# Performance work log

Measured on AMD Instinct MI355X. Metric: run time of the kernel, lower is better.

Reference implementation:

```python
import jax, jax.numpy as jnp
import numpy as np


def conv1x1(x, W, b):
    # x: [B, Cin, H, W], W: [Cout, Cin], b: [Cout] -> [B, Cout, H, W]
    return jnp.einsum('bchw,oc->bohw', x, W) + b[None, :, None, None]


def setup_inputs() -> dict:
    key = jax.random.key(0)
    ks = jax.random.split(key, 10)
    B, C, H, W = 16, 512, 64, 64
    c = C // 8  # in_ch // scale
    s_in = 1.0 / np.sqrt(C)
    s_c = 1.0 / np.sqrt(c)
    return {
        'x': jax.random.normal(ks[0], (B, C, H, W), dtype=jnp.float32),
        'Wq': jax.random.normal(ks[1], (c, C), dtype=jnp.float32) * s_in,
        'bq': jax.random.normal(ks[2], (c,), dtype=jnp.float32) * 0.01,
        'Wk': jax.random.normal(ks[3], (c, C), dtype=jnp.float32) * s_in,
        'bk': jax.random.normal(ks[4], (c,), dtype=jnp.float32) * 0.01,
        'Wv': jax.random.normal(ks[5], (c, C), dtype=jnp.float32) * s_in,
        'bv': jax.random.normal(ks[6], (c,), dtype=jnp.float32) * 0.01,
        'Wo': jax.random.normal(ks[7], (C, c), dtype=jnp.float32) * s_c,
        'bo': jax.random.normal(ks[8], (C,), dtype=jnp.float32) * 0.01,
        'gamma': jax.random.uniform(ks[9], (1,), dtype=jnp.float32),
    }


def reference(x, Wq, bq, Wk, bk, Wv, bv, Wo, bo, gamma):
    B, C, H, W = x.shape
    c = Wq.shape[0]
    N = H * W
    queries = conv1x1(x, Wq, bq).reshape(B, c, N)          # [B, c, N]
    # NOTE: original torch code does .view(-1, h*w, c): a pure reshape of the
    # contiguous [B, c, N] buffer, NOT a transpose. Reproduce exactly.
    keys = conv1x1(x, Wk, bk).reshape(B, N, c)             # [B, N, c] (reshape!)
    attn = jax.nn.softmax(jnp.einsum('bcn,bnd->bcd', queries, keys), axis=-1)  # [B, c, c]
    values = conv1x1(x, Wv, bv).reshape(B, c, N)           # [B, c, N]
    out = jnp.einsum('bcd,bdn->bcn', attn, values).reshape(B, c, H, W)
    out = conv1x1(out, Wo, bo)                             # [B, C, H, W]
    return out * gamma + x
```

## Files before the change

### kernel.cpp

```cpp
#include <hip/hip_runtime.h>

typedef unsigned short ushortT;
typedef unsigned int uintT;
typedef __attribute__((ext_vector_type(8))) short short8;
typedef __attribute__((ext_vector_type(4))) short short4v;
typedef __attribute__((ext_vector_type(4))) float float4v;

constexpr int B  = 16;
constexpr int C  = 512;
constexpr int CC = 64;
constexpr int N  = 4096;

constexpr size_t QK_OFF  = 0;
constexpr size_t S_OFF   = 8388608;
constexpr size_t VT_OFF  = 8454144;
constexpr size_t MF_OFF  = 10551296;
constexpr size_t WH_OFF  = 10813440;
constexpr size_t WL_OFF  = 10862592;
constexpr size_t WOT_OFF = 10911744;
constexpr size_t SP_OFF  = 10944512;

#define GLL(lds, g) __builtin_amdgcn_global_load_lds( \
    (const __attribute__((address_space(1))) void*)(g), \
    (__attribute__((address_space(3))) void*)(lds), 16, 0, 0)

static __device__ __forceinline__ ushortT f2bf(float f) {
    uintT u = __float_as_uint(f);
    u = (u + 0x7fffu + ((u >> 16) & 1u)) >> 16;
    return (ushortT)u;
}
static __device__ __forceinline__ float bf2f(ushortT h) {
    return __uint_as_float(((uintT)h) << 16);
}

__global__ __launch_bounds__(256) void k_prep_w(
    const float* __restrict__ Wq, const float* __restrict__ Wk,
    const float* __restrict__ Wv, const float* __restrict__ Wo,
    ushortT* __restrict__ wh, ushortT* __restrict__ wl, float* __restrict__ wot)
{
    int idx = blockIdx.x * 256 + threadIdx.x;
    if (idx < 3 * CC * C) {
        int m = idx >> 9, k = idx & 511;
        const float* W = (m < 64) ? Wq : (m < 128 ? Wk : Wv);
        float v = W[(m & 63) * C + k];
        ushortT h = f2bf(v);
        ushortT l = f2bf(v - bf2f(h));
        int kt = k >> 6, kk = k & 63;
        size_t off = ((size_t)(kt * 192 + m)) * 64 + (size_t)(((kk >> 3) ^ (m & 7)) * 8) + (kk & 7);
        wh[off] = h;
        wl[off] = l;
    } else {
        int i2 = idx - 3 * CC * C;
        int cc = i2 >> 9, co = i2 & 511;
        wot[i2] = Wo[co * CC + cc];
    }
}

__global__ __launch_bounds__(256) void k_qkv(
    const float* __restrict__ x,
    const ushortT* __restrict__ wh, const ushortT* __restrict__ wl,
    const float* __restrict__ bq, const float* __restrict__ bk,
    const float* __restrict__ bv,
    float* __restrict__ qk, ushortT* __restrict__ vt)
{
    __shared__ ushortT Ah[192 * 64];
    __shared__ ushortT Al[192 * 64];
    __shared__ ushortT Bh[2][64 * 64];
    __shared__ ushortT Bl[2][64 * 64];

    const int tid  = threadIdx.x;
    const int n0   = blockIdx.x * 64;
    const int b    = blockIdx.y;
    const int lane = tid & 63;
    const int wv   = tid >> 6;
    const int L15  = lane & 15, Lq = lane >> 4;

    const int nl  = tid & 63;
    const int kg0 = tid >> 6;

    const float* xb = x + (size_t)b * C * N + n0 + nl;

    float xr[2][8];
    float4v acc[3][4];
    const float4v vzero = {0.f, 0.f, 0.f, 0.f};
#pragma unroll
    for (int mi = 0; mi < 3; ++mi)
#pragma unroll
        for (int ni = 0; ni < 4; ++ni) acc[mi][ni] = vzero;

#pragma unroll
    for (int u = 0; u < 2; ++u) {
        const int kg = kg0 + 4 * u;
#pragma unroll
        for (int j = 0; j < 8; ++j)
            xr[u][j] = xb[(size_t)(kg * 8 + j) * N];
    }
    {
        const char* srcH = (const char*)wh;
        const char* srcL = (const char*)wl;
#pragma unroll
        for (int i = 0; i < 6; ++i) {
            int off = i * 4096 + tid * 16;
            GLL((char*)Ah + off, srcH + off);
            GLL((char*)Al + off, srcL + off);
        }
    }
#pragma unroll
    for (int u = 0; u < 2; ++u) {
        const int kg = kg0 + 4 * u;
        short8 h8, l8;
#pragma unroll
        for (int j = 0; j < 8; ++j) {
            float v = xr[u][j];
            ushortT h = f2bf(v);
            h8[j] = (short)h;
            l8[j] = (short)f2bf(v - bf2f(h));
        }
        int idx = nl * 64 + (kg ^ (nl & 7)) * 8;
        *(short8*)&Bh[0][idx] = h8;
        *(short8*)&Bl[0][idx] = l8;
    }
    __syncthreads();

    for (int kt = 0; kt < 8; ++kt) {
        const int cur = kt & 1;
        if (kt < 7) {
#pragma unroll
            for (int u = 0; u < 2; ++u) {
                const int kg = kg0 + 4 * u;
#pragma unroll
                for (int j = 0; j < 8; ++j)
                    xr[u][j] = xb[(size_t)((kt + 1) * 64 + kg * 8 + j) * N];
            }
        }
#pragma unroll
        for (int s = 0; s < 2; ++s) {
            short8 fbh[4], fbl[4];
#pragma unroll
            for (int ni = 0; ni < 4; ++ni) {
                int row = ni * 16 + L15;
                int off = row * 64 + ((4 * s + Lq) ^ (row & 7)) * 8;
                fbh[ni] = *(const short8*)&Bh[cur][off];
                fbl[ni] = *(const short8*)&Bl[cur][off];
            }
#pragma unroll
            for (int mi = 0; mi < 3; ++mi) {
                int rm = 48 * wv + mi * 16 + L15;
                int aoff = rm * 64 + ((4 * s + Lq) ^ (rm & 7)) * 8;
                short8 ah = *(const short8*)&Ah[aoff];
                short8 al = *(const short8*)&Al[aoff];
#pragma unroll
                for (int ni = 0; ni < 4; ++ni)
                    acc[mi][ni] = __builtin_amdgcn_mfma_f32_16x16x32_bf16(ah, fbh[ni], acc[mi][ni], 0, 0, 0);
#pragma unroll
                for (int ni = 0; ni < 4; ++ni)
                    acc[mi][ni] = __builtin_amdgcn_mfma_f32_16x16x32_bf16(al, fbh[ni], acc[mi][ni], 0, 0, 0);
#pragma unroll
                for (int ni = 0; ni < 4; ++ni)
                    acc[mi][ni] = __builtin_amdgcn_mfma_f32_16x16x32_bf16(ah, fbl[ni], acc[mi][ni], 0, 0, 0);
            }
        }
        __syncthreads();
        if (kt < 7) {
            const char* srcH = (const char*)wh + (size_t)(kt + 1) * 24576;
            const char* srcL = (const char*)wl + (size_t)(kt + 1) * 24576;
#pragma unroll
            for (int i = 0; i < 6; ++i) {
                int off = i * 4096 + tid * 16;
                GLL((char*)Ah + off, srcH + off);
                GLL((char*)Al + off, srcL + off);
            }
            const int nxt = cur ^ 1;
#pragma unroll
            for (int u = 0; u < 2; ++u) {
                const int kg = kg0 + 4 * u;
                short8 h8, l8;
#pragma unroll
                for (int j = 0; j < 8; ++j) {
                    float v = xr[u][j];
                    ushortT h = f2bf(v);
                    h8[j] = (short)h;
                    l8[j] = (short)f2bf(v - bf2f(h));
                }
                int idx = nl * 64 + (kg ^ (nl & 7)) * 8;
                *(short8*)&Bh[nxt][idx] = h8;
                *(short8*)&Bl[nxt][idx] = l8;
            }
            __syncthreads();
        }
    }

#pragma unroll
    for (int mi = 0; mi < 3; ++mi) {
        int rbase = 48 * wv + mi * 16;
        int type = rbase >> 6;
#pragma unroll
        for (int ni = 0; ni < 4; ++ni) {
            int col = n0 + ni * 16 + L15;
            float4v v4 = acc[mi][ni];
            if (type == 0) {
#pragma unroll
                for (int reg = 0; reg < 4; ++reg) {
                    int rl = (rbase + Lq * 4 + reg) & 63;
                    qk[((size_t)(b * 64 + rl)) * N + col] = v4[reg] + bq[rl];
                }
            } else if (type == 1) {
#pragma unroll
                for (int reg = 0; reg < 4; ++reg) {
                    int rl = (rbase + Lq * 4 + reg) & 63;
                    qk[((size_t)((16 + b) * 64 + rl)) * N + col] = v4[reg] + bk[rl];
                }
            } else {
                int rl0 = (rbase + Lq * 4) & 63;
                short4v p;
#pragma unroll
                for (int reg = 0; reg < 4; ++reg)
                    p[reg] = (short)f2bf(v4[reg] + bv[rl0 + reg]);
                size_t off = ((size_t)(b * N + col)) * 64 + (size_t)(((rl0 >> 3) ^ (col & 7)) * 8) + (rl0 & 7);
                *(short4v*)&vt[off] = p;
            }
        }
    }
}

__global__ __launch_bounds__(256) void k_logits(
    const float* __restrict__ qk, float* __restrict__ Sp)
{
    int b    = blockIdx.x;
    int part = blockIdx.y;
    __shared__ float Qs[64 * 68];
    __shared__ float Ks[64 * 64];

    const float* Qb = qk + (size_t)b * (CC * N);
    const float* Kb = qk + (size_t)(16 + b) * (CC * N);
    int tid = threadIdx.x;
    int ti = tid >> 4, tj = tid & 15;
    int i0 = ti * 4, j0 = tj * 4;
    float accl[4][4] = {};

    for (int ci = 0; ci < 2; ++ci) {
        int n0 = (part * 2 + ci) * 64;
        if (ci) __syncthreads();
        for (int t = tid; t < 1024; t += 256) {
            int i = t >> 4, c4 = (t & 15) * 4;
            *(float4*)&Qs[i * 68 + c4] = *(const float4*)&Qb[(size_t)i * N + n0 + c4];
            *(float4*)&Ks[t * 4]       = *(const float4*)&Kb[(size_t)n0 * 64 + t * 4];
        }
        __syncthreads();
        for (int nn = 0; nn < 64; ++nn) {
            float4 kv = *reinterpret_cast<const float4*>(&Ks[nn * 64 + j0]);
            float qa[4];
#pragma unroll
            for (int a = 0; a < 4; ++a) qa[a] = Qs[(i0 + a) * 68 + nn];
#pragma unroll
            for (int a = 0; a < 4; ++a) {
                accl[a][0] = fmaf(qa[a], kv.x, accl[a][0]);
                accl[a][1] = fmaf(qa[a], kv.y, accl[a][1]);
                accl[a][2] = fmaf(qa[a], kv.z, accl[a][2]);
                accl[a][3] = fmaf(qa[a], kv.w, accl[a][3]);
            }
        }
    }
    float* So = Sp + ((size_t)part * 16 + b) * (CC * CC);
#pragma unroll
    for (int a = 0; a < 4; ++a) {
        float4 v = make_float4(accl[a][0], accl[a][1], accl[a][2], accl[a][3]);
        *(float4*)&So[(i0 + a) * 64 + j0] = v;
    }
}

__global__ __launch_bounds__(256) void k_softmax_m(
    const float* __restrict__ Sp, const float* __restrict__ wot,
    ushortT* __restrict__ mf)
{
    int b = blockIdx.x, chunk = blockIdx.y;
    __shared__ float A[64 * 65];
    int tid = threadIdx.x;

    for (int t = tid; t < 1024; t += 256) {
        int r = t >> 4, c4 = (t & 15) * 4;
        size_t base = (size_t)b * (CC * CC) + r * 64 + c4;
        float4 s = *(const float4*)&Sp[base];
#pragma unroll 8
        for (int p = 1; p < 32; ++p) {
            float4 v = *(const float4*)&Sp[(size_t)p * 16 * (CC * CC) + base];
            s.x += v.x; s.y += v.y; s.z += v.z; s.w += v.w;
        }
        A[r * 65 + c4 + 0] = s.x;
        A[r * 65 + c4 + 1] = s.y;
        A[r * 65 + c4 + 2] = s.z;
        A[r * 65 + c4 + 3] = s.w;
    }
    __syncthreads();
    if (tid < 64) {
        float mx = -1e30f;
        for (int j = 0; j < 64; ++j) mx = fmaxf(mx, A[tid * 65 + j]);
        float sum = 0.f;
        for (int j = 0; j < 64; ++j) {
            float e = __expf(A[tid * 65 + j] - mx);
            A[tid * 65 + j] = e;
            sum += e;
        }
        float inv = 1.f / sum;
        for (int j = 0; j < 64; ++j) A[tid * 65 + j] *= inv;
    }
    __syncthreads();

    int co = chunk * 64 + (tid & 63);
    int e0 = (tid >> 6) * 16;
    float acc[16] = {};
    for (int cc = 0; cc < 64; ++cc) {
        float w = wot[cc * C + co];
#pragma unroll
        for (int ee = 0; ee < 16; ++ee)
            acc[ee] = fmaf(w, A[cc * 65 + e0 + ee], acc[ee]);
    }
#pragma unroll
    for (int d = 0; d < 2; ++d) {
        int c = (e0 >> 3) + d;
        uintT p0 = (uintT)f2bf(acc[d * 8 + 0]) | ((uintT)f2bf(acc[d * 8 + 1]) << 16);
        uintT p1 = (uintT)f2bf(acc[d * 8 + 2]) | ((uintT)f2bf(acc[d * 8 + 3]) << 16);
        uintT p2 = (uintT)f2bf(acc[d * 8 + 4]) | ((uintT)f2bf(acc[d * 8 + 5]) << 16);
        uintT p3 = (uintT)f2bf(acc[d * 8 + 6]) | ((uintT)f2bf(acc[d * 8 + 7]) << 16);
        uint4 pk = make_uint4(p0, p1, p2, p3);
        size_t off = ((size_t)(b * C + co)) * 64 + (size_t)((c ^ (co & 7)) * 8);
        *(uint4*)&mf[off] = pk;
    }
}

__global__ __launch_bounds__(256) void k_out(
    const ushortT* __restrict__ vt, const ushortT* __restrict__ mf,
    const float* __restrict__ x, const float* __restrict__ bo,
    const float* __restrict__ gamma, float* __restrict__ out)
{
    __shared__ ushortT As[64 * 64];
    __shared__ ushortT Bs[256 * 64];

    int b = blockIdx.x, ct = blockIdx.y, nt = blockIdx.z;
    int co0 = ct * 64, n0 = nt * 256;
    int tid = threadIdx.x;
    const char* asrc = (const char*)mf + ((size_t)(b * C + co0)) * 128;
    const char* bsrc = (const char*)vt + ((size_t)(b * N + n0)) * 128;
#pragma unroll
    for (int i = 0; i < 2; ++i) {
        int off = i * 4096 + tid * 16;
        GLL((char*)As + off, asrc + off);
    }
#pragma unroll
    for (int i = 0; i < 8; ++i) {
        int off = i * 4096 + tid * 16;
        GLL((char*)Bs + off, bsrc + off);
    }
    __syncthreads();

    int lane = tid & 63, wv = tid >> 6;
    int L15 = lane & 15, Lq = lane >> 4;
    float4v acc[4][4];
    const float4v vzero = {0.f, 0.f, 0.f, 0.f};
#pragma unroll
    for (int mi = 0; mi < 4; ++mi)
#pragma unroll
        for (int ni = 0; ni < 4; ++ni) acc[mi][ni] = vzero;

#pragma unroll
    for (int s = 0; s < 2; ++s) {
        short8 fa[4], fbm[4];
#pragma unroll
        for (int mi = 0; mi < 4; ++mi) {
            int row = wv * 64 + mi * 16 + L15;
            fa[mi] = *(const short8*)&Bs[row * 64 + ((4 * s + Lq) ^ (row & 7)) * 8];
        }
#pragma unroll
        for (int ni = 0; ni < 4; ++ni) {
            int rm = ni * 16 + L15;
            fbm[ni] = *(const short8*)&As[rm * 64 + ((4 * s + Lq) ^ (rm & 7)) * 8];
        }
#pragma unroll
        for (int mi = 0; mi < 4; ++mi)
#pragma unroll
            for (int ni = 0; ni < 4; ++ni)
                acc[mi][ni] = __builtin_amdgcn_mfma_f32_16x16x32_bf16(fa[mi], fbm[ni], acc[mi][ni], 0, 0, 0);
    }

    float g = gamma[0];
#pragma unroll
    for (int ni = 0; ni < 4; ++ni) {
        int co = co0 + ni * 16 + L15;
        float bov = bo[co];
#pragma unroll
        for (int mi = 0; mi < 4; ++mi) {
            int nbase = n0 + wv * 64 + mi * 16 + Lq * 4;
            size_t idx = ((size_t)(b * C + co)) * N + nbase;
            float4 xv = *(const float4*)&x[idx];
            float4v v4 = acc[mi][ni];
            float4 o;
            o.x = fmaf(g, v4[0] + bov, xv.x);
            o.y = fmaf(g, v4[1] + bov, xv.y);
            o.z = fmaf(g, v4[2] + bov, xv.z);
            o.w = fmaf(g, v4[3] + bov, xv.w);
            *(float4*)&out[idx] = o;
        }
    }
}

extern "C" void kernel_launch(void* const* d_in, const int* in_sizes, int n_in,
                              void* d_out, int out_size, void* d_ws, size_t ws_size,
                              hipStream_t stream)
{
    const float* x     = (const float*)d_in[0];
    const float* Wq    = (const float*)d_in[1];
    const float* bq    = (const float*)d_in[2];
    const float* Wk    = (const float*)d_in[3];
    const float* bk    = (const float*)d_in[4];
    const float* Wv    = (const float*)d_in[5];
    const float* bv    = (const float*)d_in[6];
    const float* Wo    = (const float*)d_in[7];
    const float* bo    = (const float*)d_in[8];
    const float* gamma = (const float*)d_in[9];

    float* ws   = (float*)d_ws;
    float* qk   = ws + QK_OFF;
    ushortT* vt = (ushortT*)(ws + VT_OFF);
    ushortT* mf = (ushortT*)(ws + MF_OFF);
    ushortT* wh = (ushortT*)(ws + WH_OFF);
    ushortT* wl = (ushortT*)(ws + WL_OFF);
    float* wot  = ws + WOT_OFF;
    float* Sp   = ws + SP_OFF;

    k_prep_w<<<512, 256, 0, stream>>>(Wq, Wk, Wv, Wo, wh, wl, wot);
    k_qkv<<<dim3(64, 16), 256, 0, stream>>>(x, wh, wl, bq, bk, bv, qk, vt);
    k_logits<<<dim3(16, 32), 256, 0, stream>>>(qk, Sp);
    k_softmax_m<<<dim3(16, 8), 256, 0, stream>>>(Sp, wot, mf);
    k_out<<<dim3(16, 8, 16), 256, 0, stream>>>(vt, mf, x, bo, gamma, (float*)d_out);
}
```

Measured before the change: 355.7 us.

## Load QKV weight fragments directly into registers and deepen x prefetch pipeline

```diff
diff --git a/kernel.cpp b/kernel.cpp
--- a/kernel.cpp
+++ b/kernel.cpp
@@ -46,7 +46,7 @@
         ushortT h = f2bf(v);
         ushortT l = f2bf(v - bf2f(h));
         int kt = k >> 6, kk = k & 63;
-        size_t off = ((size_t)(kt * 192 + m)) * 64 + (size_t)(((kk >> 3) ^ (m & 7)) * 8) + (kk & 7);
+        size_t off = ((size_t)(kt * 192 + m)) * 64 + kk;
         wh[off] = h;
         wl[off] = l;
     } else {
@@ -63,8 +63,6 @@
     const float* __restrict__ bv,
     float* __restrict__ qk, ushortT* __restrict__ vt)
 {
-    __shared__ ushortT Ah[192 * 64];
-    __shared__ ushortT Al[192 * 64];
     __shared__ ushortT Bh[2][64 * 64];
     __shared__ ushortT Bl[2][64 * 64];
 
@@ -80,7 +78,11 @@
 
     const float* xb = x + (size_t)b * C * N + n0 + nl;
 
+    const ushortT* wAh = wh + (size_t)(48 * wv + L15) * 64 + Lq * 8;
+    const ushortT* wAl = wl + (size_t)(48 * wv + L15) * 64 + Lq * 8;
+
     float xr[2][8];
+    short8 aH[2][3][2], aL[2][3][2];
     float4v acc[3][4];
     const float4v vzero = {0.f, 0.f, 0.f, 0.f};
 #pragma unroll
@@ -95,16 +97,14 @@
         for (int j = 0; j < 8; ++j)
             xr[u][j] = xb[(size_t)(kg * 8 + j) * N];
     }
-    {
-        const char* srcH = (const char*)wh;
-        const char* srcL = (const char*)wl;
-#pragma unroll
-        for (int i = 0; i < 6; ++i) {
-            int off = i * 4096 + tid * 16;
-            GLL((char*)Ah + off, srcH + off);
-            GLL((char*)Al + off, srcL + off);
-        }
-    }
+#pragma unroll
+    for (int mi = 0; mi < 3; ++mi)
+#pragma unroll
+        for (int s = 0; s < 2; ++s) {
+            size_t o = (size_t)(mi * 16) * 64 + s * 32;
+            aH[0][mi][s] = *(const short8*)&wAh[o];
+            aL[0][mi][s] = *(const short8*)&wAl[o];
+        }
 #pragma unroll
     for (int u = 0; u < 2; ++u) {
         const int kg = kg0 + 4 * u;
@@ -120,18 +120,28 @@
         *(short8*)&Bh[0][idx] = h8;
         *(short8*)&Bl[0][idx] = l8;
     }
+#pragma unroll
+    for (int u = 0; u < 2; ++u) {
+        const int kg = kg0 + 4 * u;
+#pragma unroll
+        for (int j = 0; j < 8; ++j)
+            xr[u][j] = xb[(size_t)(64 + kg * 8 + j) * N];
+    }
     __syncthreads();
 
+#pragma unroll
     for (int kt = 0; kt < 8; ++kt) {
         const int cur = kt & 1;
+        const int nb  = cur ^ 1;
         if (kt < 7) {
 #pragma unroll
-            for (int u = 0; u < 2; ++u) {
-                const int kg = kg0 + 4 * u;
-#pragma unroll
-                for (int j = 0; j < 8; ++j)
-                    xr[u][j] = xb[(size_t)((kt + 1) * 64 + kg * 8 + j) * N];
-            }
+            for (int mi = 0; mi < 3; ++mi)
+#pragma unroll
+                for (int s = 0; s < 2; ++s) {
+                    size_t o = (size_t)((kt + 1) * 192 + mi * 16) * 64 + s * 32;
+                    aH[nb][mi][s] = *(const short8*)&wAh[o];
+                    aL[nb][mi][s] = *(const short8*)&wAl[o];
+                }
         }
 #pragma unroll
         for (int s = 0; s < 2; ++s) {
@@ -143,12 +153,11 @@
                 fbh[ni] = *(const short8*)&Bh[cur][off];
                 fbl[ni] = *(const short8*)&Bl[cur][off];
             }
+            __builtin_amdgcn_s_setprio(1);
 #pragma unroll
             for (int mi = 0; mi < 3; ++mi) {
-                int rm = 48 * wv + mi * 16 + L15;
-                int aoff = rm * 64 + ((4 * s + Lq) ^ (rm & 7)) * 8;
-                short8 ah = *(const short8*)&Ah[aoff];
-                short8 al = *(const short8*)&Al[aoff];
+                short8 ah = aH[cur][mi][s];
+                short8 al = aL[cur][mi][s];
 #pragma unroll
                 for (int ni = 0; ni < 4; ++ni)
                     acc[mi][ni] = __builtin_amdgcn_mfma_f32_16x16x32_bf16(ah, fbh[ni], acc[mi][ni], 0, 0, 0);
@@ -159,18 +168,9 @@
                 for (int ni = 0; ni < 4; ++ni)
                     acc[mi][ni] = __builtin_amdgcn_mfma_f32_16x16x32_bf16(ah, fbl[ni], acc[mi][ni], 0, 0, 0);
             }
-        }
-        __syncthreads();
+            __builtin_amdgcn_s_setprio(0);
+        }
         if (kt < 7) {
-            const char* srcH = (const char*)wh + (size_t)(kt + 1) * 24576;
-            const char* srcL = (const char*)wl + (size_t)(kt + 1) * 24576;
-#pragma unroll
-            for (int i = 0; i < 6; ++i) {
-                int off = i * 4096 + tid * 16;
-                GLL((char*)Ah + off, srcH + off);
-                GLL((char*)Al + off, srcL + off);
-            }
-            const int nxt = cur ^ 1;
 #pragma unroll
             for (int u = 0; u < 2; ++u) {
                 const int kg = kg0 + 4 * u;
@@ -183,11 +183,20 @@
                     l8[j] = (short)f2bf(v - bf2f(h));
                 }
                 int idx = nl * 64 + (kg ^ (nl & 7)) * 8;
-                *(short8*)&Bh[nxt][idx] = h8;
-                *(short8*)&Bl[nxt][idx] = l8;
-            }
-            __syncthreads();
-        }
+                *(short8*)&Bh[nb][idx] = h8;
+                *(short8*)&Bl[nb][idx] = l8;
+            }
+            if (kt < 6) {
+#pragma unroll
+                for (int u = 0; u < 2; ++u) {
+                    const int kg = kg0 + 4 * u;
+#pragma unroll
+                    for (int j = 0; j < 8; ++j)
+                        xr[u][j] = xb[(size_t)((kt + 2) * 64 + kg * 8 + j) * N];
+                }
+            }
+        }
+        __syncthreads();
     }
 
 #pragma unroll
```

Measured after the change: 370.9 us. 1.04x slower.

## Stream low-part weights from global into registers and shrink LDS buffers

Applied to the files above, without the earlier changes.

```diff
diff --git a/kernel.cpp b/kernel.cpp
--- a/kernel.cpp
+++ b/kernel.cpp
@@ -46,9 +46,9 @@
         ushortT h = f2bf(v);
         ushortT l = f2bf(v - bf2f(h));
         int kt = k >> 6, kk = k & 63;
-        size_t off = ((size_t)(kt * 192 + m)) * 64 + (size_t)(((kk >> 3) ^ (m & 7)) * 8) + (kk & 7);
-        wh[off] = h;
-        wl[off] = l;
+        size_t base = ((size_t)(kt * 192 + m)) * 64;
+        wh[base + (size_t)(((kk >> 3) ^ (m & 7)) * 8) + (kk & 7)] = h;
+        wl[base + kk] = l;
     } else {
         int i2 = idx - 3 * CC * C;
         int cc = i2 >> 9, co = i2 & 511;
@@ -64,9 +64,8 @@
     float* __restrict__ qk, ushortT* __restrict__ vt)
 {
     __shared__ ushortT Ah[192 * 64];
-    __shared__ ushortT Al[192 * 64];
     __shared__ ushortT Bh[2][64 * 64];
-    __shared__ ushortT Bl[2][64 * 64];
+    __shared__ ushortT Bl[64 * 64];
 
     const int tid  = threadIdx.x;
     const int n0   = blockIdx.x * 64;
@@ -80,6 +79,8 @@
 
     const float* xb = x + (size_t)b * C * N + n0 + nl;
 
+    const ushortT* wAl = wl + (size_t)(48 * wv + L15) * 64 + Lq * 8;
+
     float xr[2][8];
     float4v acc[3][4];
     const float4v vzero = {0.f, 0.f, 0.f, 0.f};
@@ -97,12 +98,10 @@
     }
     {
         const char* srcH = (const char*)wh;
-        const char* srcL = (const char*)wl;
 #pragma unroll
         for (int i = 0; i < 6; ++i) {
             int off = i * 4096 + tid * 16;
             GLL((char*)Ah + off, srcH + off);
-            GLL((char*)Al + off, srcL + off);
         }
     }
 #pragma unroll
@@ -118,21 +117,26 @@
         }
         int idx = nl * 64 + (kg ^ (nl & 7)) * 8;
         *(short8*)&Bh[0][idx] = h8;
-        *(short8*)&Bl[0][idx] = l8;
+        *(short8*)&Bl[idx]    = l8;
+    }
+#pragma unroll
+    for (int u = 0; u < 2; ++u) {
+        const int kg = kg0 + 4 * u;
+#pragma unroll
+        for (int j = 0; j < 8; ++j)
+            xr[u][j] = xb[(size_t)(64 + kg * 8 + j) * N];
     }
     __syncthreads();
 
     for (int kt = 0; kt < 8; ++kt) {
         const int cur = kt & 1;
-        if (kt < 7) {
-#pragma unroll
-            for (int u = 0; u < 2; ++u) {
-                const int kg = kg0 + 4 * u;
-#pragma unroll
-                for (int j = 0; j < 8; ++j)
-                    xr[u][j] = xb[(size_t)((kt + 1) * 64 + kg * 8 + j) * N];
-            }
-        }
+        short8 alr[3][2];
+#pragma unroll
+        for (int mi = 0; mi < 3; ++mi)
+#pragma unroll
+            for (int s = 0; s < 2; ++s)
+                alr[mi][s] = *(const short8*)&wAl[(size_t)(kt * 192 + mi * 16) * 64 + s * 32];
+
 #pragma unroll
         for (int s = 0; s < 2; ++s) {
             short8 fbh[4], fbl[4];
@@ -141,34 +145,33 @@
                 int row = ni * 16 + L15;
                 int off = row * 64 + ((4 * s + Lq) ^ (row & 7)) * 8;
                 fbh[ni] = *(const short8*)&Bh[cur][off];
-                fbl[ni] = *(const short8*)&Bl[cur][off];
+                fbl[ni] = *(const short8*)&Bl[off];
             }
 #pragma unroll
             for (int mi = 0; mi < 3; ++mi) {
                 int rm = 48 * wv + mi * 16 + L15;
-                int aoff = rm * 64 + ((4 * s + Lq) ^ (rm & 7)) * 8;
-                short8 ah = *(const short8*)&Ah[aoff];
-                short8 al = *(const short8*)&Al[aoff];
+                short8 ah = *(const short8*)&Ah[rm * 64 + ((4 * s + Lq) ^ (rm & 7)) * 8];
 #pragma unroll
                 for (int ni = 0; ni < 4; ++ni)
                     acc[mi][ni] = __builtin_amdgcn_mfma_f32_16x16x32_bf16(ah, fbh[ni], acc[mi][ni], 0, 0, 0);
 #pragma unroll
                 for (int ni = 0; ni < 4; ++ni)
-                    acc[mi][ni] = __builtin_amdgcn_mfma_f32_16x16x32_bf16(al, fbh[ni], acc[mi][ni], 0, 0, 0);
+                    acc[mi][ni] = __builtin_amdgcn_mfma_f32_16x16x32_bf16(ah, fbl[ni], acc[mi][ni], 0, 0, 0);
+            }
+#pragma unroll
+            for (int mi = 0; mi < 3; ++mi) {
 #pragma unroll
                 for (int ni = 0; ni < 4; ++ni)
-                    acc[mi][ni] = __builtin_amdgcn_mfma_f32_16x16x32_bf16(ah, fbl[ni], acc[mi][ni], 0, 0, 0);
+                    acc[mi][ni] = __builtin_amdgcn_mfma_f32_16x16x32_bf16(alr[mi][s], fbh[ni], acc[mi][ni], 0, 0, 0);
             }
         }
         __syncthreads();
         if (kt < 7) {
             const char* srcH = (const char*)wh + (size_t)(kt + 1) * 24576;
-            const char* srcL = (const char*)wl + (size_t)(kt + 1) * 24576;
 #pragma unroll
             for (int i = 0; i < 6; ++i) {
                 int off = i * 4096 + tid * 16;
                 GLL((char*)Ah + off, srcH + off);
-                GLL((char*)Al + off, srcL + off);
             }
             const int nxt = cur ^ 1;
 #pragma unroll
@@ -184,7 +187,16 @@
                 }
                 int idx = nl * 64 + (kg ^ (nl & 7)) * 8;
                 *(short8*)&Bh[nxt][idx] = h8;
-                *(short8*)&Bl[nxt][idx] = l8;
+                *(short8*)&Bl[idx]      = l8;
+            }
+            if (kt < 6) {
+#pragma unroll
+                for (int u = 0; u < 2; ++u) {
+                    const int kg = kg0 + 4 * u;
+#pragma unroll
+                    for (int j = 0; j < 8; ++j)
+                        xr[u][j] = xb[(size_t)((kt + 2) * 64 + kg * 8 + j) * N];
+                }
             }
             __syncthreads();
         }
```

Result: no change. 362.3 us (+1.9%).

## Load QKV weight fragments directly from global into registers, dropping LDS staging

Applied to the files above, without the earlier changes.

```diff
diff --git a/kernel.cpp b/kernel.cpp
--- a/kernel.cpp
+++ b/kernel.cpp
@@ -46,7 +46,7 @@
         ushortT h = f2bf(v);
         ushortT l = f2bf(v - bf2f(h));
         int kt = k >> 6, kk = k & 63;
-        size_t off = ((size_t)(kt * 192 + m)) * 64 + (size_t)(((kk >> 3) ^ (m & 7)) * 8) + (kk & 7);
+        size_t off = ((size_t)(kt * 192 + m)) * 64 + kk;
         wh[off] = h;
         wl[off] = l;
     } else {
@@ -63,8 +63,6 @@
     const float* __restrict__ bv,
     float* __restrict__ qk, ushortT* __restrict__ vt)
 {
-    __shared__ ushortT Ah[192 * 64];
-    __shared__ ushortT Al[192 * 64];
     __shared__ ushortT Bh[2][64 * 64];
     __shared__ ushortT Bl[2][64 * 64];
 
@@ -80,6 +78,9 @@
 
     const float* xb = x + (size_t)b * C * N + n0 + nl;
 
+    const ushortT* wAh = wh + (size_t)(48 * wv + L15) * 64 + Lq * 8;
+    const ushortT* wAl = wl + (size_t)(48 * wv + L15) * 64 + Lq * 8;
+
     float xr[2][8];
     float4v acc[3][4];
     const float4v vzero = {0.f, 0.f, 0.f, 0.f};
@@ -94,16 +95,6 @@
 #pragma unroll
         for (int j = 0; j < 8; ++j)
             xr[u][j] = xb[(size_t)(kg * 8 + j) * N];
-    }
-    {
-        const char* srcH = (const char*)wh;
-        const char* srcL = (const char*)wl;
-#pragma unroll
-        for (int i = 0; i < 6; ++i) {
-            int off = i * 4096 + tid * 16;
-            GLL((char*)Ah + off, srcH + off);
-            GLL((char*)Al + off, srcL + off);
-        }
     }
 #pragma unroll
     for (int u = 0; u < 2; ++u) {
@@ -124,6 +115,16 @@
 
     for (int kt = 0; kt < 8; ++kt) {
         const int cur = kt & 1;
+        const int nxt = cur ^ 1;
+        short8 ahr[3][2], alr[3][2];
+#pragma unroll
+        for (int mi = 0; mi < 3; ++mi)
+#pragma unroll
+            for (int s = 0; s < 2; ++s) {
+                size_t o = (size_t)(kt * 192 + mi * 16) * 64 + s * 32;
+                ahr[mi][s] = *(const short8*)&wAh[o];
+                alr[mi][s] = *(const short8*)&wAl[o];
+            }
         if (kt < 7) {
 #pragma unroll
             for (int u = 0; u < 2; ++u) {
@@ -145,32 +146,20 @@
             }
 #pragma unroll
             for (int mi = 0; mi < 3; ++mi) {
-                int rm = 48 * wv + mi * 16 + L15;
-                int aoff = rm * 64 + ((4 * s + Lq) ^ (rm & 7)) * 8;
-                short8 ah = *(const short8*)&Ah[aoff];
-                short8 al = *(const short8*)&Al[aoff];
+                short8 ah = ahr[mi][s];
+                short8 al = alr[mi][s];
 #pragma unroll
                 for (int ni = 0; ni < 4; ++ni)
                     acc[mi][ni] = __builtin_amdgcn_mfma_f32_16x16x32_bf16(ah, fbh[ni], acc[mi][ni], 0, 0, 0);
 #pragma unroll
                 for (int ni = 0; ni < 4; ++ni)
+                    acc[mi][ni] = __builtin_amdgcn_mfma_f32_16x16x32_bf16(ah, fbl[ni], acc[mi][ni], 0, 0, 0);
+#pragma unroll
+                for (int ni = 0; ni < 4; ++ni)
                     acc[mi][ni] = __builtin_amdgcn_mfma_f32_16x16x32_bf16(al, fbh[ni], acc[mi][ni], 0, 0, 0);
-#pragma unroll
-                for (int ni = 0; ni < 4; ++ni)
-                    acc[mi][ni] = __builtin_amdgcn_mfma_f32_16x16x32_bf16(ah, fbl[ni], acc[mi][ni], 0, 0, 0);
-            }
-        }
-        __syncthreads();
+            }
+        }
         if (kt < 7) {
-            const char* srcH = (const char*)wh + (size_t)(kt + 1) * 24576;
-            const char* srcL = (const char*)wl + (size_t)(kt + 1) * 24576;
-#pragma unroll
-            for (int i = 0; i < 6; ++i) {
-                int off = i * 4096 + tid * 16;
-                GLL((char*)Ah + off, srcH + off);
-                GLL((char*)Al + off, srcL + off);
-            }
-            const int nxt = cur ^ 1;
 #pragma unroll
             for (int u = 0; u < 2; ++u) {
                 const int kg = kg0 + 4 * u;
@@ -186,8 +175,8 @@
                 *(short8*)&Bh[nxt][idx] = h8;
                 *(short8*)&Bl[nxt][idx] = l8;
             }
-            __syncthreads();
-        }
+        }
+        __syncthreads();
     }
 
 #pragma unroll
```

New measurement: 369.3 us. +3.8%, slower.
